# Kernel optimization log

Measured on AMD Instinct MI355X. Metric: run time of the kernel, lower is better.

Reference implementation:

```python
import jax, jax.numpy as jnp
import numpy as np

B, H, W, C = 2, 64, 64, 512
GROUPS = 32
EPS = 1e-5


def group_norm(x, gamma, beta):
    b, h, w, c = x.shape
    xg = x.reshape(b, h, w, GROUPS, c // GROUPS)
    mu = xg.mean(axis=(1, 2, 4), keepdims=True)
    var = xg.var(axis=(1, 2, 4), keepdims=True)
    xn = ((xg - mu) * jax.lax.rsqrt(var + EPS)).reshape(b, h, w, c)
    return xn * gamma + beta


def setup_inputs() -> dict:
    key = jax.random.key(0)
    ks = jax.random.split(key, 12)
    wscale = 0.02
    inputs = jax.random.normal(ks[0], (B, H, W, C), jnp.float32)
    gamma = jnp.ones((C,), jnp.float32)
    beta = jnp.zeros((C,), jnp.float32)
    Wq = jax.random.normal(ks[1], (C, C), jnp.float32) * wscale
    bq = jnp.zeros((C,), jnp.float32)
    Wk = jax.random.normal(ks[2], (C, C), jnp.float32) * wscale
    bk = jnp.zeros((C,), jnp.float32)
    Wv = jax.random.normal(ks[3], (C, C), jnp.float32) * wscale
    bv = jnp.zeros((C,), jnp.float32)
    Wp = jax.random.normal(ks[4], (C, C), jnp.float32) * wscale
    bp = jnp.zeros((C,), jnp.float32)
    return {"inputs": inputs, "gamma": gamma, "beta": beta,
            "Wq": Wq, "bq": bq, "Wk": Wk, "bk": bk,
            "Wv": Wv, "bv": bv, "Wp": Wp, "bp": bp}


def reference(inputs, gamma, beta, Wq, bq, Wk, bk, Wv, bv, Wp, bp):
    b, h, w, c = inputs.shape
    x = group_norm(inputs, gamma, beta)
    # QKV projections on [b, h, w, c], flatten spatial to sequence hw
    q = (x @ Wq + bq).reshape(b, h * w, c)
    k = (x @ Wk + bk).reshape(b, h * w, c)
    v = (x @ Wv + bv).reshape(b, h * w, c)
    scale = 1.0 / jnp.sqrt(jnp.asarray(c, q.dtype))
    # y[b,i,j] = <q_i, k_j> / sqrt(c); softmax over keys j (last axis, keras default)
    attn = jax.nn.softmax(jnp.einsum('bqc,bkc->bqk', q, k) * scale, axis=-1)
    # out_i = sum_j attn[i,j] * v_j  (matches v @ y^T in the original)
    o = jnp.einsum('bqk,bkc->bqc', attn, v).reshape(b, h, w, c)
    return (o @ Wp + bp) + inputs
```

## Files before the change

kernel.cpp:

```cpp
#include <hip/hip_runtime.h>
#include <hip/hip_bf16.h>
#include <cstddef>


typedef __bf16 bf16;
typedef __attribute__((ext_vector_type(8))) __bf16 bf16x8;
typedef __attribute__((ext_vector_type(4))) __bf16 bf16x4;
typedef __attribute__((ext_vector_type(4))) float f32x4;

#define SEQ   4096
#define CCH   512
#define NBAT  2

__global__ __launch_bounds__(256) void gn_stats(const float* __restrict__ x,
                                                float* __restrict__ stats) {
    int bg = blockIdx.x;
    int b = bg >> 5, g = bg & 31;
    const float* base = x + (size_t)b * SEQ * CCH + g * 16;
    float s = 0.f, ss = 0.f;
    for (int i = threadIdx.x; i < 16384; i += 256) {
        int sp = i >> 2, q = i & 3;
        float4 v = *(const float4*)(base + (size_t)sp * CCH + q * 4);
        s  += v.x + v.y + v.z + v.w;
        ss += v.x * v.x + v.y * v.y + v.z * v.z + v.w * v.w;
    }
    #pragma unroll
    for (int o = 32; o > 0; o >>= 1) { s += __shfl_down(s, o); ss += __shfl_down(ss, o); }
    __shared__ float red[2][4];
    int wave = threadIdx.x >> 6, lane = threadIdx.x & 63;
    if (lane == 0) { red[0][wave] = s; red[1][wave] = ss; }
    __syncthreads();
    if (threadIdx.x == 0) {
        float S  = red[0][0] + red[0][1] + red[0][2] + red[0][3];
        float SS = red[1][0] + red[1][1] + red[1][2] + red[1][3];
        float mu = S * (1.f / 65536.f);
        float var = SS * (1.f / 65536.f) - mu * mu;
        stats[bg * 2]     = mu;
        stats[bg * 2 + 1] = rsqrtf(var + 1e-5f);
    }
}

__global__ __launch_bounds__(256) void gn_apply(const float* __restrict__ x,
                                                const float* __restrict__ stats,
                                                const float* __restrict__ gamma,
                                                const float* __restrict__ beta,
                                                bf16* __restrict__ xn) {
    size_t idx = (size_t)blockIdx.x * 256 + threadIdx.x;
    int c4 = (int)(idx & 127);
    size_t sb = idx >> 7;
    int b = (int)(sb >> 12);
    int g = c4 >> 2;
    int bg = b * 32 + g;
    float mu = stats[bg * 2], rs = stats[bg * 2 + 1];
    float4 v  = ((const float4*)x)[idx];
    float4 gm = ((const float4*)gamma)[c4];
    float4 bt = ((const float4*)beta)[c4];
    bf16x4 o;
    o[0] = (bf16)((v.x - mu) * rs * gm.x + bt.x);
    o[1] = (bf16)((v.y - mu) * rs * gm.y + bt.y);
    o[2] = (bf16)((v.z - mu) * rs * gm.z + bt.z);
    o[3] = (bf16)((v.w - mu) * rs * gm.w + bt.w);
    ((bf16x4*)xn)[idx] = o;
}

__global__ __launch_bounds__(256) void wtrans(const float* __restrict__ Wq,
                                              const float* __restrict__ Wk,
                                              const float* __restrict__ Wv,
                                              const float* __restrict__ Wp,
                                              bf16* __restrict__ WqkvT,
                                              bf16* __restrict__ WpT) {
    __shared__ float tile[32][33];
    int z = blockIdx.z;
    const float* W = (z == 0) ? Wq : (z == 1) ? Wk : (z == 2) ? Wv : Wp;
    int tx = threadIdx.x & 31, ty = threadIdx.x >> 5;
    int k0 = blockIdx.x * 32;
    int n0 = blockIdx.y * 32;
    #pragma unroll
    for (int i = ty; i < 32; i += 8)
        tile[i][tx] = W[(size_t)(k0 + i) * CCH + n0 + tx];
    __syncthreads();
    bf16* dst = (z < 3) ? (WqkvT + (size_t)z * CCH * CCH) : WpT;
    #pragma unroll
    for (int i = ty; i < 32; i += 8)
        dst[(size_t)(n0 + i) * CCH + k0 + tx] = (bf16)tile[tx][i];
}

__global__ __launch_bounds__(256) void pack_bias(const float* __restrict__ bq,
                                                 const float* __restrict__ bk,
                                                 const float* __restrict__ bv,
                                                 float* __restrict__ dst) {
    int i = blockIdx.x * 256 + threadIdx.x;
    if (i < 512)       dst[i] = bq[i];
    else if (i < 1024) dst[i] = bk[i - 512];
    else if (i < 1536) dst[i] = bv[i - 1024];
}

__global__ __launch_bounds__(256) void vtrans(const bf16* __restrict__ qkv,
                                              bf16* __restrict__ vT) {
    __shared__ bf16 tile[32][33];
    int b = blockIdx.z;
    int s0 = blockIdx.x * 32, c0 = blockIdx.y * 32;
    int tx = threadIdx.x & 31, ty = threadIdx.x >> 5;
    #pragma unroll
    for (int i = ty; i < 32; i += 8)
        tile[i][tx] = qkv[(size_t)(b * SEQ + s0 + i) * 1536 + 1024 + c0 + tx];
    __syncthreads();
    #pragma unroll
    for (int i = ty; i < 32; i += 8)
        vT[((size_t)b * CCH + c0 + i) * SEQ + s0 + tx] = tile[tx][i];
}

__global__ __launch_bounds__(256) void lsum_reduce(const float* __restrict__ lsum,
                                                   float* __restrict__ linv) {
    int idx = blockIdx.x * 256 + threadIdx.x;
    int b = idx >> 12, row = idx & 4095;
    const float* p = lsum + (long long)b * 64 * SEQ + row;
    float s = 0.f;
    #pragma unroll
    for (int i = 0; i < 64; ++i) s += p[(long long)i * SEQ];
    linv[idx] = 1.f / s;
}

template <int EPI, int BN>
__global__ __launch_bounds__(256, 2) void gemm2(
    const bf16* __restrict__ A, long long aBatch, int lda,
    const bf16* __restrict__ Bt, long long bBatch, int ldb,
    void* __restrict__ Cout, long long cBatch, int ldc,
    int K, int bkmask, float scale,
    const float* __restrict__ bias, const float* __restrict__ resid,
    float* __restrict__ lsum, long long lsumBatch,
    const float* __restrict__ linv) {
    constexpr int JN = BN / 32;
    __shared__ __align__(16) bf16 As[128 * 64];
    __shared__ __align__(16) bf16 Bs[BN * 64];
    __shared__ float lrow[128];
    const int tid = threadIdx.x;
    const int lane = tid & 63;
    const int wave = tid >> 6;

    int zb = blockIdx.z, kc = 0;
    if constexpr (EPI == 2) { kc = zb & 1; zb >>= 1; }
    const long long m0 = (long long)blockIdx.x * 128;
    const long long n0 = (long long)blockIdx.y * BN;
    const bf16* Ab = A + (long long)zb * aBatch + (EPI == 2 ? (long long)kc * 2048 : 0);
    const bf16* Bb = Bt + (long long)zb * bBatch + (EPI == 2 ? (long long)kc * 2048 : 0);

    if constexpr (EPI == 2) {
        if (tid < 128) lrow[tid] = linv[(long long)zb * SEQ + m0 + tid];
    }

    const int wm = (wave & 1) * 64;
    const int wn = (wave >> 1) * (BN / 2);
    const int fm = lane & 15;
    const int q4 = lane >> 4;

    f32x4 acc[4][JN];
    #pragma unroll
    for (int i = 0; i < 4; ++i)
        #pragma unroll
        for (int j = 0; j < JN; ++j)
            acc[i][j] = (f32x4){0.f, 0.f, 0.f, 0.f};

    const int srow = tid >> 3;
    const int schunk = (tid & 7) ^ (srow & 7);

    for (int k0 = 0; k0 < K; k0 += 64) {
        const int kA = k0 + schunk * 8;
        const int kB = (k0 & bkmask) + schunk * 8;
        #pragma unroll
        for (int cb = 0; cb < 4; ++cb) {
            const bf16* g = Ab + (m0 + cb * 32 + srow) * (long long)lda + kA;
            __builtin_amdgcn_global_load_lds((const __attribute__((address_space(1))) void*)g,
                                             (__attribute__((address_space(3))) void*)&As[cb * 2048 + tid * 8], 16, 0, 0);
        }
        #pragma unroll
        for (int cb = 0; cb < BN / 32; ++cb) {
            const bf16* g = Bb + (n0 + cb * 32 + srow) * (long long)ldb + kB;
            __builtin_amdgcn_global_load_lds((const __attribute__((address_space(1))) void*)g,
                                             (__attribute__((address_space(3))) void*)&Bs[cb * 2048 + tid * 8], 16, 0, 0);
        }
        __syncthreads();
        #pragma unroll
        for (int kcc = 0; kcc < 2; ++kcc) {
            bf16x8 fa[4], fb[JN];
            #pragma unroll
            for (int i = 0; i < 4; ++i) {
                const int row = wm + i * 16 + fm;
                const int sw = ((kcc * 4 + q4) ^ (fm & 7)) * 8;
                fa[i] = *(const bf16x8*)&As[row * 64 + sw];
            }
            #pragma unroll
            for (int j = 0; j < JN; ++j) {
                const int row = wn + j * 16 + fm;
                const int sw = ((kcc * 4 + q4) ^ (fm & 7)) * 8;
                fb[j] = *(const bf16x8*)&Bs[row * 64 + sw];
            }
            #pragma unroll
            for (int i = 0; i < 4; ++i)
                #pragma unroll
                for (int j = 0; j < JN; ++j)
                    acc[i][j] = __builtin_amdgcn_mfma_f32_16x16x32_bf16(fa[i], fb[j], acc[i][j], 0, 0, 0);
        }
        __syncthreads();
    }

    const int col = lane & 15;
    const int rowb = (lane >> 4) * 4;

    if constexpr (EPI == 1) {
        bf16* Pb = (bf16*)Cout + (long long)zb * cBatch;
        float* lsw = lsum + (long long)zb * lsumBatch
                   + ((long long)blockIdx.y * 2 + (wave >> 1)) * SEQ;
        #pragma unroll
        for (int i = 0; i < 4; ++i) {
            float rs[4] = {0.f, 0.f, 0.f, 0.f};
            long long mg = m0 + wm + i * 16 + rowb;
            #pragma unroll
            for (int j = 0; j < JN; ++j) {
                long long ng = n0 + wn + j * 16 + col;
                #pragma unroll
                for (int r = 0; r < 4; ++r) {
                    float e = __expf(acc[i][j][r] * scale);
                    rs[r] += e;
                    Pb[(mg + r) * (long long)ldc + ng] = (bf16)e;
                }
            }
            #pragma unroll
            for (int r = 0; r < 4; ++r) {
                rs[r] += __shfl_xor(rs[r], 1);
                rs[r] += __shfl_xor(rs[r], 2);
                rs[r] += __shfl_xor(rs[r], 4);
                rs[r] += __shfl_xor(rs[r], 8);
            }
            if (col == 0) {
                #pragma unroll
                for (int r = 0; r < 4; ++r) lsw[mg + r] = rs[r];
            }
        }
    } else {
        #pragma unroll
        for (int i = 0; i < 4; ++i) {
            #pragma unroll
            for (int j = 0; j < JN; ++j) {
                long long mg = m0 + wm + i * 16 + rowb;
                long long ng = n0 + wn + j * 16 + col;
                #pragma unroll
                for (int r = 0; r < 4; ++r) {
                    float v = acc[i][j][r];
                    long long m = mg + r;
                    if constexpr (EPI == 0) {
                        ((bf16*)Cout)[m * (long long)ldc + ng] = (bf16)(v + bias[ng]);
                    } else if constexpr (EPI == 2) {
                        float inv = lrow[(int)(m - m0)];
                        ((bf16*)Cout)[(long long)zb * cBatch + m * (long long)ldc
                                      + kc * 512 + ng] = (bf16)(v * inv);
                    } else {
                        ((float*)Cout)[m * (long long)ldc + ng] =
                            v + bias[ng] + resid[m * CCH + ng];
                    }
                }
            }
        }
    }
}

extern "C" void kernel_launch(void* const* d_in, const int* in_sizes, int n_in,
                              void* d_out, int out_size, void* d_ws, size_t ws_size,
                              hipStream_t stream) {
    const float* x     = (const float*)d_in[0];
    const float* gamma = (const float*)d_in[1];
    const float* beta  = (const float*)d_in[2];
    const float* Wq    = (const float*)d_in[3];
    const float* bq    = (const float*)d_in[4];
    const float* Wk    = (const float*)d_in[5];
    const float* bk    = (const float*)d_in[6];
    const float* Wv    = (const float*)d_in[7];
    const float* bv    = (const float*)d_in[8];
    const float* Wp    = (const float*)d_in[9];
    const float* bp    = (const float*)d_in[10];
    float* out = (float*)d_out;

    constexpr size_t OFF_STATS = 0;
    constexpr size_t OFF_BIAS  = 1024;
    constexpr size_t OFF_WQKVT = 8192;
    constexpr size_t OFF_WPT   = 1581056;
    constexpr size_t OFF_XN    = 2105344;
    constexpr size_t OFF_LSUM  = OFF_XN;
    constexpr size_t OFF_LINV  = OFF_XN + 2097152;
    constexpr size_t OFF_QKV   = 10493952;
    constexpr size_t OFF_O2    = OFF_QKV;
    constexpr size_t OFF_VT    = 35659776;
    constexpr size_t OFF_P     = 44048384;
    constexpr size_t NEED_FULL = OFF_P + (size_t)NBAT * SEQ * SEQ * 2;

    char* ws = (char*)d_ws;
    float* stats   = (float*)(ws + OFF_STATS);
    float* biasQKV = (float*)(ws + OFF_BIAS);
    bf16*  WqkvT   = (bf16*)(ws + OFF_WQKVT);
    bf16*  WpT     = (bf16*)(ws + OFF_WPT);
    bf16*  xn      = (bf16*)(ws + OFF_XN);
    float* lsum    = (float*)(ws + OFF_LSUM);
    float* linv    = (float*)(ws + OFF_LINV);
    bf16*  qkv     = (bf16*)(ws + OFF_QKV);
    bf16*  o2      = (bf16*)(ws + OFF_O2);
    bf16*  vT      = (bf16*)(ws + OFF_VT);
    bf16*  P       = (bf16*)(ws + OFF_P);

    const float scale = 0.044194173824159216f;
    const int NOMASK = 0x7FFFFFFF;

    gn_stats<<<64, 256, 0, stream>>>(x, stats);
    gn_apply<<<4096, 256, 0, stream>>>(x, stats, gamma, beta, xn);
    wtrans<<<dim3(16, 16, 4), 256, 0, stream>>>(Wq, Wk, Wv, Wp, WqkvT, WpT);
    pack_bias<<<6, 256, 0, stream>>>(bq, bk, bv, biasQKV);

    gemm2<0, 128><<<dim3(64, 12, 1), 256, 0, stream>>>(
        xn, 0, CCH, WqkvT, 0, CCH, qkv, 0, 1536,
        CCH, NOMASK, 1.f, biasQKV, nullptr, nullptr, 0, nullptr);
    vtrans<<<dim3(128, 16, NBAT), 256, 0, stream>>>(qkv, vT);

    if (ws_size >= NEED_FULL) {
        gemm2<1, 128><<<dim3(32, 32, NBAT), 256, 0, stream>>>(
            qkv, (long long)SEQ * 1536, 1536, qkv + 512, (long long)SEQ * 1536, 1536,
            P, (long long)SEQ * SEQ, SEQ,
            CCH, NOMASK, scale, nullptr, nullptr, lsum, 64LL * SEQ, nullptr);
        lsum_reduce<<<32, 256, 0, stream>>>(lsum, linv);
        gemm2<2, 128><<<dim3(32, 4, NBAT * 2), 256, 0, stream>>>(
            P, (long long)SEQ * SEQ, SEQ, vT, (long long)CCH * SEQ, SEQ,
            o2, (long long)SEQ * 1024, 1024,
            2048, NOMASK, 1.f, nullptr, nullptr, nullptr, 0, linv);
    } else {
        for (int b = 0; b < NBAT; ++b) {
            const bf16* qb = qkv + (long long)b * SEQ * 1536;
            gemm2<1, 128><<<dim3(32, 32, 1), 256, 0, stream>>>(
                qb, 0, 1536, qb + 512, 0, 1536, P, 0, SEQ,
                CCH, NOMASK, scale, nullptr, nullptr,
                lsum + (long long)b * 64 * SEQ, 0, nullptr);
            lsum_reduce<<<16, 256, 0, stream>>>(lsum + (long long)b * 64 * SEQ,
                                                linv + (long long)b * SEQ);
            gemm2<2, 128><<<dim3(32, 4, 2), 256, 0, stream>>>(
                P, 0, SEQ, vT + (long long)b * CCH * SEQ, 0, SEQ,
                o2 + (long long)b * SEQ * 1024, 0, 1024,
                2048, NOMASK, 1.f, nullptr, nullptr, nullptr, 0,
                linv + (long long)b * SEQ);
        }
    }

    gemm2<3, 64><<<dim3(64, 8, 1), 256, 0, stream>>>(
        o2, 0, 1024, WpT, 0, CCH, out, 0, CCH,
        1024, 511, 1.f, bp, x, nullptr, 0, nullptr);
}
```

Measured before the change: 261.3 us.

## Merge small prep kernels and fold vtrans and lsum reduction into GEMMs

```diff
diff --git a/kernel.cpp b/kernel.cpp
--- a/kernel.cpp
+++ b/kernel.cpp
@@ -12,31 +12,56 @@
 #define CCH   512
 #define NBAT  2
 
-__global__ __launch_bounds__(256) void gn_stats(const float* __restrict__ x,
-                                                float* __restrict__ stats) {
-    int bg = blockIdx.x;
-    int b = bg >> 5, g = bg & 31;
-    const float* base = x + (size_t)b * SEQ * CCH + g * 16;
-    float s = 0.f, ss = 0.f;
-    for (int i = threadIdx.x; i < 16384; i += 256) {
-        int sp = i >> 2, q = i & 3;
-        float4 v = *(const float4*)(base + (size_t)sp * CCH + q * 4);
-        s  += v.x + v.y + v.z + v.w;
-        ss += v.x * v.x + v.y * v.y + v.z * v.z + v.w * v.w;
-    }
-    #pragma unroll
-    for (int o = 32; o > 0; o >>= 1) { s += __shfl_down(s, o); ss += __shfl_down(ss, o); }
-    __shared__ float red[2][4];
-    int wave = threadIdx.x >> 6, lane = threadIdx.x & 63;
-    if (lane == 0) { red[0][wave] = s; red[1][wave] = ss; }
-    __syncthreads();
-    if (threadIdx.x == 0) {
-        float S  = red[0][0] + red[0][1] + red[0][2] + red[0][3];
-        float SS = red[1][0] + red[1][1] + red[1][2] + red[1][3];
-        float mu = S * (1.f / 65536.f);
-        float var = SS * (1.f / 65536.f) - mu * mu;
-        stats[bg * 2]     = mu;
-        stats[bg * 2 + 1] = rsqrtf(var + 1e-5f);
+__global__ __launch_bounds__(256) void prep(
+    const float* __restrict__ x,
+    const float* __restrict__ Wq, const float* __restrict__ Wk,
+    const float* __restrict__ Wv, const float* __restrict__ Wp,
+    const float* __restrict__ bq, const float* __restrict__ bk,
+    const float* __restrict__ bv,
+    float* __restrict__ stats, bf16* __restrict__ WqkvT,
+    bf16* __restrict__ WpT, float* __restrict__ biasQKV) {
+    const int bid = blockIdx.x;
+    if (bid < 512) {
+        int bg = bid >> 3, c = bid & 7;
+        int b = bg >> 5, g = bg & 31;
+        const float* base = x + (size_t)b * SEQ * CCH + g * 16;
+        float s = 0.f, ss = 0.f;
+        for (int i = threadIdx.x; i < 2048; i += 256) {
+            int sp = c * 512 + (i >> 2), q = i & 3;
+            float4 v = *(const float4*)(base + (size_t)sp * CCH + q * 4);
+            s  += v.x + v.y + v.z + v.w;
+            ss += v.x * v.x + v.y * v.y + v.z * v.z + v.w * v.w;
+        }
+        #pragma unroll
+        for (int o = 32; o > 0; o >>= 1) { s += __shfl_down(s, o); ss += __shfl_down(ss, o); }
+        __shared__ float red[2][4];
+        int wave = threadIdx.x >> 6, lane = threadIdx.x & 63;
+        if (lane == 0) { red[0][wave] = s; red[1][wave] = ss; }
+        __syncthreads();
+        if (threadIdx.x == 0) {
+            atomicAdd(&stats[bg * 2],     red[0][0] + red[0][1] + red[0][2] + red[0][3]);
+            atomicAdd(&stats[bg * 2 + 1], red[1][0] + red[1][1] + red[1][2] + red[1][3]);
+        }
+    } else if (bid < 1536) {
+        __shared__ float tile[32][33];
+        int w = bid - 512;
+        int z = w >> 8, rest = w & 255;
+        int k0 = (rest >> 4) * 32, n0 = (rest & 15) * 32;
+        const float* W = (z == 0) ? Wq : (z == 1) ? Wk : (z == 2) ? Wv : Wp;
+        int tx = threadIdx.x & 31, ty = threadIdx.x >> 5;
+        #pragma unroll
+        for (int i = ty; i < 32; i += 8)
+            tile[i][tx] = W[(size_t)(k0 + i) * CCH + n0 + tx];
+        __syncthreads();
+        bf16* dst = (z < 3) ? (WqkvT + (size_t)z * CCH * CCH) : WpT;
+        #pragma unroll
+        for (int i = ty; i < 32; i += 8)
+            dst[(size_t)(n0 + i) * CCH + k0 + tx] = (bf16)tile[tx][i];
+    } else {
+        for (int i = threadIdx.x; i < 1536; i += 256) {
+            float v = (i < 512) ? bq[i] : (i < 1024) ? bk[i - 512] : bv[i - 1024];
+            biasQKV[i] = v;
+        }
     }
 }
 
@@ -51,7 +76,9 @@
     int b = (int)(sb >> 12);
     int g = c4 >> 2;
     int bg = b * 32 + g;
-    float mu = stats[bg * 2], rs = stats[bg * 2 + 1];
+    float S = stats[bg * 2], SS = stats[bg * 2 + 1];
+    float mu = S * (1.f / 65536.f);
+    float rs = rsqrtf(SS * (1.f / 65536.f) - mu * mu + 1e-5f);
     float4 v  = ((const float4*)x)[idx];
     float4 gm = ((const float4*)gamma)[c4];
     float4 bt = ((const float4*)beta)[c4];
@@ -63,90 +90,41 @@
     ((bf16x4*)xn)[idx] = o;
 }
 
-__global__ __launch_bounds__(256) void wtrans(const float* __restrict__ Wq,
-                                              const float* __restrict__ Wk,
-                                              const float* __restrict__ Wv,
-                                              const float* __restrict__ Wp,
-                                              bf16* __restrict__ WqkvT,
-                                              bf16* __restrict__ WpT) {
-    __shared__ float tile[32][33];
-    int z = blockIdx.z;
-    const float* W = (z == 0) ? Wq : (z == 1) ? Wk : (z == 2) ? Wv : Wp;
-    int tx = threadIdx.x & 31, ty = threadIdx.x >> 5;
-    int k0 = blockIdx.x * 32;
-    int n0 = blockIdx.y * 32;
-    #pragma unroll
-    for (int i = ty; i < 32; i += 8)
-        tile[i][tx] = W[(size_t)(k0 + i) * CCH + n0 + tx];
-    __syncthreads();
-    bf16* dst = (z < 3) ? (WqkvT + (size_t)z * CCH * CCH) : WpT;
-    #pragma unroll
-    for (int i = ty; i < 32; i += 8)
-        dst[(size_t)(n0 + i) * CCH + k0 + tx] = (bf16)tile[tx][i];
-}
-
-__global__ __launch_bounds__(256) void pack_bias(const float* __restrict__ bq,
-                                                 const float* __restrict__ bk,
-                                                 const float* __restrict__ bv,
-                                                 float* __restrict__ dst) {
-    int i = blockIdx.x * 256 + threadIdx.x;
-    if (i < 512)       dst[i] = bq[i];
-    else if (i < 1024) dst[i] = bk[i - 512];
-    else if (i < 1536) dst[i] = bv[i - 1024];
-}
-
-__global__ __launch_bounds__(256) void vtrans(const bf16* __restrict__ qkv,
-                                              bf16* __restrict__ vT) {
-    __shared__ bf16 tile[32][33];
-    int b = blockIdx.z;
-    int s0 = blockIdx.x * 32, c0 = blockIdx.y * 32;
-    int tx = threadIdx.x & 31, ty = threadIdx.x >> 5;
-    #pragma unroll
-    for (int i = ty; i < 32; i += 8)
-        tile[i][tx] = qkv[(size_t)(b * SEQ + s0 + i) * 1536 + 1024 + c0 + tx];
-    __syncthreads();
-    #pragma unroll
-    for (int i = ty; i < 32; i += 8)
-        vT[((size_t)b * CCH + c0 + i) * SEQ + s0 + tx] = tile[tx][i];
-}
-
-__global__ __launch_bounds__(256) void lsum_reduce(const float* __restrict__ lsum,
-                                                   float* __restrict__ linv) {
-    int idx = blockIdx.x * 256 + threadIdx.x;
-    int b = idx >> 12, row = idx & 4095;
-    const float* p = lsum + (long long)b * 64 * SEQ + row;
-    float s = 0.f;
-    #pragma unroll
-    for (int i = 0; i < 64; ++i) s += p[(long long)i * SEQ];
-    linv[idx] = 1.f / s;
-}
-
 template <int EPI, int BN>
-__global__ __launch_bounds__(256, 2) void gemm2(
+__device__ __forceinline__ void gemm2_body(
+    int bxi, int byi, int bzi,
     const bf16* __restrict__ A, long long aBatch, int lda,
     const bf16* __restrict__ Bt, long long bBatch, int ldb,
     void* __restrict__ Cout, long long cBatch, int ldc,
     int K, int bkmask, float scale,
     const float* __restrict__ bias, const float* __restrict__ resid,
-    float* __restrict__ lsum, long long lsumBatch,
-    const float* __restrict__ linv) {
+    float* __restrict__ lsum, long long lsumBatch) {
     constexpr int JN = BN / 32;
     __shared__ __align__(16) bf16 As[128 * 64];
     __shared__ __align__(16) bf16 Bs[BN * 64];
+    __shared__ float lscr[256];
     __shared__ float lrow[128];
     const int tid = threadIdx.x;
     const int lane = tid & 63;
     const int wave = tid >> 6;
 
-    int zb = blockIdx.z, kc = 0;
+    int zb = bzi, kc = 0;
     if constexpr (EPI == 2) { kc = zb & 1; zb >>= 1; }
-    const long long m0 = (long long)blockIdx.x * 128;
-    const long long n0 = (long long)blockIdx.y * BN;
+    const long long m0 = (long long)bxi * 128;
+    const long long n0 = (long long)byi * BN;
     const bf16* Ab = A + (long long)zb * aBatch + (EPI == 2 ? (long long)kc * 2048 : 0);
     const bf16* Bb = Bt + (long long)zb * bBatch + (EPI == 2 ? (long long)kc * 2048 : 0);
 
     if constexpr (EPI == 2) {
-        if (tid < 128) lrow[tid] = linv[(long long)zb * SEQ + m0 + tid];
+        const float* lsb = lsum + (long long)zb * lsumBatch + m0;
+        const int row = tid & 127, h = tid >> 7;
+        float s = 0.f;
+        #pragma unroll
+        for (int p = 0; p < 32; ++p)
+            s += lsb[(long long)(h * 32 + p) * SEQ + row];
+        lscr[tid] = s;
+        __syncthreads();
+        if (tid < 128) lrow[tid] = 1.f / (lscr[tid] + lscr[tid + 128]);
     }
 
     const int wm = (wave & 1) * 64;
@@ -210,7 +188,7 @@
     if constexpr (EPI == 1) {
         bf16* Pb = (bf16*)Cout + (long long)zb * cBatch;
         float* lsw = lsum + (long long)zb * lsumBatch
-                   + ((long long)blockIdx.y * 2 + (wave >> 1)) * SEQ;
+                   + ((long long)byi * 2 + (wave >> 1)) * SEQ;
         #pragma unroll
         for (int i = 0; i < 4; ++i) {
             float rs[4] = {0.f, 0.f, 0.f, 0.f};
@@ -264,6 +242,59 @@
     }
 }
 
+template <int EPI, int BN>
+__global__ __launch_bounds__(256, 2) void gemm2(
+    const bf16* __restrict__ A, long long aBatch, int lda,
+    const bf16* __restrict__ Bt, long long bBatch, int ldb,
+    void* __restrict__ Cout, long long cBatch, int ldc,
+    int K, int bkmask, float scale,
+    const float* __restrict__ bias, const float* __restrict__ resid,
+    float* __restrict__ lsum, long long lsumBatch) {
+    gemm2_body<EPI, BN>(blockIdx.x, blockIdx.y, blockIdx.z,
+                        A, aBatch, lda, Bt, bBatch, ldb, Cout, cBatch, ldc,
+                        K, bkmask, scale, bias, resid, lsum, lsumBatch);
+}
+
+__device__ __forceinline__ void vtrans_body(const bf16* __restrict__ qkv,
+                                            bf16* __restrict__ vT,
+                                            int b, int s0, int c0) {
+    __shared__ bf16 tile[64][65];
+    const int tx = threadIdx.x & 63;
+    const int w = threadIdx.x >> 6;
+    #pragma unroll
+    for (int i = 0; i < 16; ++i) {
+        int row = w + i * 4;
+        tile[row][tx] = qkv[((size_t)b * SEQ + s0 + row) * 1536 + 1024 + c0 + tx];
+    }
+    __syncthreads();
+    #pragma unroll
+    for (int i = 0; i < 16; ++i) {
+        int row = w + i * 4;
+        vT[((size_t)b * CCH + c0 + row) * SEQ + s0 + tx] = tile[tx][row];
+    }
+}
+
+__global__ __launch_bounds__(256, 2) void qk_vtrans(
+    const bf16* __restrict__ qkv, bf16* __restrict__ vT,
+    bf16* __restrict__ P, float* __restrict__ lsum,
+    float scale, int vtBlocks,
+    long long qkBatch, long long pBatch, long long lsumBatch) {
+    const int bid = blockIdx.x;
+    if (bid < vtBlocks) {
+        int b = bid >> 9;
+        int r = bid & 511;
+        vtrans_body(qkv, vT, b, (r >> 3) * 64, (r & 7) * 64);
+    } else {
+        int q = bid - vtBlocks;
+        int bz = q >> 10;
+        int r = q & 1023;
+        gemm2_body<1, 128>(r >> 5, r & 31, bz,
+                           qkv, qkBatch, 1536, qkv + 512, qkBatch, 1536,
+                           P, pBatch, SEQ, CCH, 0x7FFFFFFF, scale,
+                           nullptr, nullptr, lsum, lsumBatch);
+    }
+}
+
 extern "C" void kernel_launch(void* const* d_in, const int* in_sizes, int n_in,
                               void* d_out, int out_size, void* d_ws, size_t ws_size,
                               hipStream_t stream) {
@@ -286,7 +317,6 @@
     constexpr size_t OFF_WPT   = 1581056;
     constexpr size_t OFF_XN    = 2105344;
     constexpr size_t OFF_LSUM  = OFF_XN;
-    constexpr size_t OFF_LINV  = OFF_XN + 2097152;
     constexpr size_t OFF_QKV   = 10493952;
     constexpr size_t OFF_O2    = OFF_QKV;
     constexpr size_t OFF_VT    = 35659776;
@@ -300,7 +330,6 @@
     bf16*  WpT     = (bf16*)(ws + OFF_WPT);
     bf16*  xn      = (bf16*)(ws + OFF_XN);
     float* lsum    = (float*)(ws + OFF_LSUM);
-    float* linv    = (float*)(ws + OFF_LINV);
     bf16*  qkv     = (bf16*)(ws + OFF_QKV);
     bf16*  o2      = (bf16*)(ws + OFF_O2);
     bf16*  vT      = (bf16*)(ws + OFF_VT);
@@ -309,44 +338,37 @@
     const float scale = 0.044194173824159216f;
     const int NOMASK = 0x7FFFFFFF;
 
-    gn_stats<<<64, 256, 0, stream>>>(x, stats);
+    hipMemsetAsync(ws + OFF_STATS, 0, 512, stream);
+    prep<<<1537, 256, 0, stream>>>(x, Wq, Wk, Wv, Wp, bq, bk, bv,
+                                   stats, WqkvT, WpT, biasQKV);
     gn_apply<<<4096, 256, 0, stream>>>(x, stats, gamma, beta, xn);
-    wtrans<<<dim3(16, 16, 4), 256, 0, stream>>>(Wq, Wk, Wv, Wp, WqkvT, WpT);
-    pack_bias<<<6, 256, 0, stream>>>(bq, bk, bv, biasQKV);
-
     gemm2<0, 128><<<dim3(64, 12, 1), 256, 0, stream>>>(
         xn, 0, CCH, WqkvT, 0, CCH, qkv, 0, 1536,
-        CCH, NOMASK, 1.f, biasQKV, nullptr, nullptr, 0, nullptr);
-    vtrans<<<dim3(128, 16, NBAT), 256, 0, stream>>>(qkv, vT);
+        CCH, NOMASK, 1.f, biasQKV, nullptr, nullptr, 0);
 
     if (ws_size >= NEED_FULL) {
-        gemm2<1, 128><<<dim3(32, 32, NBAT), 256, 0, stream>>>(
-            qkv, (long long)SEQ * 1536, 1536, qkv + 512, (long long)SEQ * 1536, 1536,
-            P, (long long)SEQ * SEQ, SEQ,
-            CCH, NOMASK, scale, nullptr, nullptr, lsum, 64LL * SEQ, nullptr);
-        lsum_reduce<<<32, 256, 0, stream>>>(lsum, linv);
+        qk_vtrans<<<3072, 256, 0, stream>>>(
+            qkv, vT, P, lsum, scale, 1024,
+            (long long)SEQ * 1536, (long long)SEQ * SEQ, 64LL * SEQ);
         gemm2<2, 128><<<dim3(32, 4, NBAT * 2), 256, 0, stream>>>(
             P, (long long)SEQ * SEQ, SEQ, vT, (long long)CCH * SEQ, SEQ,
             o2, (long long)SEQ * 1024, 1024,
-            2048, NOMASK, 1.f, nullptr, nullptr, nullptr, 0, linv);
+            2048, NOMASK, 1.f, nullptr, nullptr, lsum, 64LL * SEQ);
     } else {
         for (int b = 0; b < NBAT; ++b) {
             const bf16* qb = qkv + (long long)b * SEQ * 1536;
-            gemm2<1, 128><<<dim3(32, 32, 1), 256, 0, stream>>>(
-                qb, 0, 1536, qb + 512, 0, 1536, P, 0, SEQ,
-                CCH, NOMASK, scale, nullptr, nullptr,
-                lsum + (long long)b * 64 * SEQ, 0, nullptr);
-            lsum_reduce<<<16, 256, 0, stream>>>(lsum + (long long)b * 64 * SEQ,
-                                                linv + (long long)b * SEQ);
+            qk_vtrans<<<1536, 256, 0, stream>>>(
+                qb, vT + (long long)b * CCH * SEQ, P,
+                lsum + (long long)b * 64 * SEQ, scale, 512, 0, 0, 0);
             gemm2<2, 128><<<dim3(32, 4, 2), 256, 0, stream>>>(
                 P, 0, SEQ, vT + (long long)b * CCH * SEQ, 0, SEQ,
                 o2 + (long long)b * SEQ * 1024, 0, 1024,
-                2048, NOMASK, 1.f, nullptr, nullptr, nullptr, 0,
-                linv + (long long)b * SEQ);
+                2048, NOMASK, 1.f, nullptr, nullptr,
+                lsum + (long long)b * 64 * SEQ, 0);
         }
     }
 
     gemm2<3, 64><<<dim3(64, 8, 1), 256, 0, stream>>>(
         o2, 0, 1024, WpT, 0, CCH, out, 0, CCH,
-        1024, 511, 1.f, bp, x, nullptr, 0, nullptr);
-}
+        1024, 511, 1.f, bp, x, nullptr, 0);
+}
```

After: 220.8 us. -15.5%, faster.
